# Performance work log

Measured on AMD Instinct MI355X. Metric: run time of the kernel, lower is better.

The kernel has to match this reference:

```python
import jax, jax.numpy as jnp
import numpy as np

RADIUS_IN, RADIUS_OUT, NSAMPLE = 0.4, 0.8, 32
SCENE = 10.0  # cube edge length for point coordinates


def setup_inputs() -> dict:
    key = jax.random.key(0)
    k1, k2, k3 = jax.random.split(key, 3)
    B, N, NP, C = 2, 16384, 4096, 64
    xyz = jax.random.uniform(k1, (B, N, 3), dtype=jnp.float32) * SCENE
    new_xyz = jax.random.uniform(k2, (B, NP, 3), dtype=jnp.float32) * SCENE
    features = jax.random.normal(k3, (B, C, N), dtype=jnp.float32)
    return {"xyz": xyz, "new_xyz": new_xyz, "features": features}


def ball_query_dilated(xyz, new_xyz, min_r, max_r, nsample):
    # xyz: (B,N,3), new_xyz: (B,P,3) -> idx: (B,P,nsample) int32
    N = xyz.shape[1]
    d2 = jnp.sum((new_xyz[:, :, None, :] - xyz[:, None, :, :]) ** 2, axis=-1)  # (B,P,N)
    mask = (d2 >= min_r * min_r) & (d2 < max_r * max_r)
    ar = jnp.arange(N, dtype=jnp.int32)
    # valid points keep their index; invalid pushed after all valid ones, in order
    sort_key = jnp.where(mask, ar, ar + N)
    _, idx_sorted = jax.lax.top_k(-sort_key, nsample)  # first nsample in-range point indices
    cnt = jnp.sum(mask, axis=-1)  # (B,P)
    slot_valid = jnp.arange(nsample, dtype=cnt.dtype)[None, None, :] < cnt[:, :, None]
    # CUDA kernel fills all slots with the first found index; if none found idx stays 0
    # (when cnt==0, idx_sorted[...,0] == 0 since key N is the minimum), so this matches.
    idx = jnp.where(slot_valid, idx_sorted, idx_sorted[:, :, :1])
    return idx.astype(jnp.int32)


def group(features, idx):
    # features: (B,C,N), idx: (B,P,S) -> (B,C,P,S)
    return jax.vmap(lambda f, i: f[:, i])(features, idx)


def reference(xyz, new_xyz, features):
    idx = ball_query_dilated(xyz, new_xyz, RADIUS_IN, RADIUS_OUT, NSAMPLE)
    xyz_t = jnp.transpose(xyz, (0, 2, 1))  # (B,3,N)
    grouped_xyz = group(xyz_t, idx) - jnp.transpose(new_xyz, (0, 2, 1))[:, :, :, None]
    grouped_features = group(features, idx)
    new_features = jnp.concatenate([grouped_xyz, grouped_features], axis=1)  # (B,3+C,P,S)
    return new_features
```

## Files before the change

kernel.cpp:

```cpp
#include <hip/hip_runtime.h>
#include <hip/hip_bf16.h>

#define BB 2
#define NN 16384
#define NP 4096
#define CC 64
#define SS 32
#define NCH (3 + CC)

#define NSUB 32
#define SUBN (NN / NSUB)

__global__ void __launch_bounds__(256) pack_xyz_kernel(
    const float* __restrict__ xyz, float4* __restrict__ xyz4)
{
    int i = blockIdx.x * 256 + threadIdx.x;
    if (i < BB * NN) {
        float4 v;
        v.x = xyz[3 * i + 0];
        v.y = xyz[3 * i + 1];
        v.z = xyz[3 * i + 2];
        v.w = 0.0f;
        xyz4[i] = v;
    }
}

__global__ void __launch_bounds__(256) transpose_feat_kernel(
    const float* __restrict__ f, float* __restrict__ ft)
{
    __shared__ float tile[64 * 65];
    const int b  = blockIdx.y;
    const int n0 = blockIdx.x * 64;
    const int t  = threadIdx.x;
    const int tn  = t & 63;
    const int tc4 = t >> 6;
#pragma unroll
    for (int r = 0; r < 16; ++r) {
        int c = r * 4 + tc4;
        tile[c * 65 + tn] = f[((b * CC + c) << 14) + n0 + tn];
    }
    __syncthreads();
#pragma unroll
    for (int r = 0; r < 16; ++r) {
        int nl = r * 4 + tc4;
        ft[((b << 14) + n0 + nl) * CC + tn] = tile[tn * 65 + nl];
    }
}

__global__ void __launch_bounds__(256) query_kernel(
    const float4* __restrict__ xyz4, const float* __restrict__ new_xyz,
    unsigned short* __restrict__ part, unsigned char* __restrict__ cntp)
{
#pragma clang fp contract(off)
    __shared__ float4 pts_s[SUBN];
    const int t   = threadIdx.x;
    const int sub = blockIdx.y;
    const int q   = blockIdx.x * 256 + t;
    const int b   = q >> 12;

    const float RMIN2 = (float)(0.4 * 0.4);
    const float RMAX2 = (float)(0.8 * 0.8);

    const float4* __restrict__ pts = xyz4 + (b << 14) + sub * SUBN;
#pragma unroll
    for (int i = 0; i < SUBN / 256; ++i)
        pts_s[i * 256 + t] = pts[i * 256 + t];
    __syncthreads();

    const float qx = new_xyz[q * 3 + 0];
    const float qy = new_xyz[q * 3 + 1];
    const float qz = new_xyz[q * 3 + 2];

    unsigned short* __restrict__ mypart = part + (q * NSUB + sub) * SS;
    const int base = sub * SUBN;

    int cnt = 0;
#pragma unroll 8
    for (int j = 0; j < SUBN; ++j) {
        float4 pt = pts_s[j];
        float dx = pt.x - qx;
        float dy = pt.y - qy;
        float dz = pt.z - qz;
        float dx2 = dx * dx;
        float dy2 = dy * dy;
        float dz2 = dz * dz;
        float d2 = (dx2 + dy2) + dz2;
        bool valid = (d2 >= RMIN2) && (d2 < RMAX2);
        if (valid && cnt < SS) {
            mypart[cnt] = (unsigned short)(base + j);
            cnt++;
        }
    }
    cntp[q * NSUB + sub] = (unsigned char)cnt;
}

__global__ void __launch_bounds__(256) merge_kernel(
    const unsigned short* __restrict__ part, const unsigned char* __restrict__ cntp,
    int* __restrict__ idxg)
{
    const int lane = threadIdx.x & 63;
    const int w    = threadIdx.x >> 6;
    const int q    = blockIdx.x * 4 + w;

    int c = (lane < NSUB) ? (int)cntp[q * NSUB + lane] : 0;

    int off = c;
#pragma unroll
    for (int d = 1; d < 64; d <<= 1) {
        int v = __shfl_up(off, d);
        if (lane >= d) off += v;
    }
    int total = __shfl(off, 63);
    if (total > SS) total = SS;
    off -= c;

    const unsigned short* __restrict__ p = part + (q * NSUB + lane) * SS;
    int firstval = (c > 0) ? (int)p[0] : 0;
    unsigned long long m = __ballot(c > 0);
    int first = 0;
    if (m) {
        int fl = __ffsll((unsigned long long)m) - 1;
        first = __shfl(firstval, fl);
    }

    int* __restrict__ o = idxg + q * SS;
    for (int j = 0; j < c; ++j) {
        int s = off + j;
        if (s < SS) o[s] = (int)p[j];
    }
    if (lane < SS && lane >= total) o[lane] = first;
}

__global__ void __launch_bounds__(256) group_kernel(
    const float4* __restrict__ xyz4, const float* __restrict__ new_xyz,
    const float* __restrict__ ft, const int* __restrict__ idxg,
    float* __restrict__ out)
{
    __shared__ float tile[4][SS * 65];
    const int w    = threadIdx.x >> 6;
    const int lane = threadIdx.x & 63;
    const int q    = blockIdx.x * 4 + w;
    const int b    = q >> 12;
    const int p    = q & (NP - 1);
    const int s    = lane & 31;

    const int idxv = idxg[q * SS + s];

    float4 pt = xyz4[(b << 14) + idxv];
    float q0 = new_xyz[q * 3 + 0];
    float q1 = new_xyz[q * 3 + 1];
    float q2 = new_xyz[q * 3 + 2];
    if (lane < 32) {
        out[((b * NCH + 0) * NP + p) * SS + s] = pt.x - q0;
        out[((b * NCH + 1) * NP + p) * SS + s] = pt.y - q1;
        out[((b * NCH + 2) * NP + p) * SS + s] = pt.z - q2;
    }

    float* tl = tile[w];
#pragma unroll 8
    for (int s2 = 0; s2 < SS; ++s2) {
        int n = __shfl(idxv, s2);
        tl[s2 * 65 + lane] = ft[(((b << 14) + n) << 6) + lane];
    }
    __syncthreads();
    const int chalf = lane >> 5;
#pragma unroll 8
    for (int cp = 0; cp < 32; ++cp) {
        int cch = cp * 2 + chalf;
        out[((b * NCH + 3 + cch) * NP + p) * SS + s] = tl[s * 65 + cch];
    }
}

extern "C" void kernel_launch(void* const* d_in, const int* in_sizes, int n_in,
                              void* d_out, int out_size, void* d_ws, size_t ws_size,
                              hipStream_t stream)
{
    const float* xyz      = (const float*)d_in[0];
    const float* new_xyz  = (const float*)d_in[1];
    const float* features = (const float*)d_in[2];
    float* out = (float*)d_out;

    char* ws = (char*)d_ws;
    float4*         xyz4 = (float4*)(ws);
    float*          ft   = (float*)(ws + 524288);
    unsigned short* part = (unsigned short*)(ws + 8912896);
    unsigned char*  cntp = (unsigned char*)(ws + 25690112);
    int*            idxg = (int*)(ws + 25952256);

    hipLaunchKernelGGL(pack_xyz_kernel, dim3((BB * NN) / 256), dim3(256), 0, stream,
                       xyz, xyz4);
    hipLaunchKernelGGL(transpose_feat_kernel, dim3(NN / 64, BB), dim3(256), 0, stream,
                       features, ft);
    hipLaunchKernelGGL(query_kernel, dim3((BB * NP) / 256, NSUB), dim3(256), 0, stream,
                       xyz4, new_xyz, part, cntp);
    hipLaunchKernelGGL(merge_kernel, dim3((BB * NP) / 4), dim3(256), 0, stream,
                       part, cntp, idxg);
    hipLaunchKernelGGL(group_kernel, dim3((BB * NP) / 4), dim3(256), 0, stream,
                       xyz4, new_xyz, ft, idxg, out);
}
```

Baseline: 164.5 us.

## Batch ball-query distance tests into bitmasks and restage group tile in halves

```diff
diff --git a/kernel.cpp b/kernel.cpp
--- a/kernel.cpp
+++ b/kernel.cpp
@@ -60,6 +60,8 @@
 
     const float RMIN2 = (float)(0.4 * 0.4);
     const float RMAX2 = (float)(0.8 * 0.8);
+    const unsigned ULO = __float_as_uint(RMIN2);
+    const unsigned URNG = __float_as_uint(RMAX2) - ULO;
 
     const float4* __restrict__ pts = xyz4 + (b << 14) + sub * SUBN;
 #pragma unroll
@@ -75,20 +77,33 @@
     const int base = sub * SUBN;
 
     int cnt = 0;
-#pragma unroll 8
-    for (int j = 0; j < SUBN; ++j) {
-        float4 pt = pts_s[j];
-        float dx = pt.x - qx;
-        float dy = pt.y - qy;
-        float dz = pt.z - qz;
-        float dx2 = dx * dx;
-        float dy2 = dy * dy;
-        float dz2 = dz * dz;
-        float d2 = (dx2 + dy2) + dz2;
-        bool valid = (d2 >= RMIN2) && (d2 < RMAX2);
-        if (valid && cnt < SS) {
-            mypart[cnt] = (unsigned short)(base + j);
-            cnt++;
+    for (int j0 = 0; j0 < SUBN; j0 += 8) {
+        float4 P[8];
+#pragma unroll
+        for (int k = 0; k < 8; ++k) P[k] = pts_s[j0 + k];
+        unsigned m = 0;
+#pragma unroll
+        for (int k = 0; k < 8; ++k) {
+            float dx = P[k].x - qx;
+            float dy = P[k].y - qy;
+            float dz = P[k].z - qz;
+            float dx2 = dx * dx;
+            float dy2 = dy * dy;
+            float dz2 = dz * dz;
+            float d2 = (dx2 + dy2) + dz2;
+            unsigned ud = __float_as_uint(d2);
+            bool valid = (ud - ULO) < URNG;
+            m |= valid ? (1u << k) : 0u;
+        }
+        if (m) {
+            do {
+                int k = __ffs(m) - 1;
+                m &= m - 1;
+                if (cnt < SS) {
+                    mypart[cnt] = (unsigned short)(base + j0 + k);
+                    cnt++;
+                }
+            } while (m);
         }
     }
     cntp[q * NSUB + sub] = (unsigned char)cnt;
@@ -136,7 +151,7 @@
     const float* __restrict__ ft, const int* __restrict__ idxg,
     float* __restrict__ out)
 {
-    __shared__ float tile[4][SS * 65];
+    __shared__ float tile[4][16 * 66];
     const int w    = threadIdx.x >> 6;
     const int lane = threadIdx.x & 63;
     const int q    = blockIdx.x * 4 + w;
@@ -157,17 +172,23 @@
     }
 
     float* tl = tile[w];
-#pragma unroll 8
-    for (int s2 = 0; s2 < SS; ++s2) {
-        int n = __shfl(idxv, s2);
-        tl[s2 * 65 + lane] = ft[(((b << 14) + n) << 6) + lane];
-    }
-    __syncthreads();
-    const int chalf = lane >> 5;
-#pragma unroll 8
-    for (int cp = 0; cp < 32; ++cp) {
-        int cch = cp * 2 + chalf;
-        out[((b * NCH + 3 + cch) * NP + p) * SS + s] = tl[s * 65 + cch];
+    const float* __restrict__ ftb = ft + (b << 14) * CC;
+    const int sl = lane & 15;
+    const int cq = lane >> 4;
+#pragma unroll
+    for (int h = 0; h < 2; ++h) {
+#pragma unroll
+        for (int s2 = 0; s2 < 16; ++s2) {
+            int n = __shfl(idxv, h * 16 + s2);
+            tl[s2 * 66 + lane] = ftb[(n << 6) + lane];
+        }
+        asm volatile("s_waitcnt lgkmcnt(0)" ::: "memory");
+#pragma unroll
+        for (int cp = 0; cp < 16; ++cp) {
+            int ch = cp * 4 + cq;
+            out[((b * NCH + 3 + ch) * NP + p) * SS + h * 16 + sl] = tl[sl * 66 + ch];
+        }
+        asm volatile("s_waitcnt lgkmcnt(0)" ::: "memory");
     }
 }
 
```

Measured after the change: 158.0 us. 1.04x faster.
